# Kernel tuning notes

Measured on AMD Instinct MI355X. Metric: run time of the kernel, lower is better.

The kernel has to match this reference:

```python
import jax, jax.numpy as jnp
import numpy as np

B, S, E, D = 8, 2048, 512, 512  # batch, seq (mesh edges), elem_size, embd_size


def setup_inputs() -> dict:
    key = jax.random.key(0)
    ks = jax.random.split(key, 5)
    scale = 1.0 / np.sqrt(E)
    return {
        "x": jax.random.normal(ks[0], (B, S, E), dtype=jnp.float32),
        "Wq": jax.random.normal(ks[1], (E, D), dtype=jnp.float32) * scale,
        "bq": jax.random.normal(ks[2], (D,), dtype=jnp.float32) * 0.01,
        "Wk": jax.random.normal(ks[3], (E, D), dtype=jnp.float32) * scale,
        "bk": jax.random.normal(ks[4], (D,), dtype=jnp.float32) * 0.01,
    }


def reference(x, Wq, bq, Wk, bk):
    elem_size = x.shape[-1]
    q = jax.nn.relu(x @ Wq + bq)              # [B,S,D]
    k = jax.nn.relu(x @ Wk + bk)              # [B,S,D]
    scores = jnp.einsum("bqd,bkd->bqk", q, k) / (elem_size ** 0.5)  # [B,S,S]
    # nn.Softmax(dim=1): normalize over the QUERY axis (column-wise softmax)
    attn = jax.nn.softmax(scores, axis=1)
    new_values = jnp.einsum("bqk,bke->bqe", attn, x)  # V = raw x (use_V=False)
    return x + new_values                     # residual connection
```

## Files before the change

### kernel.cpp

```cpp
#include <hip/hip_runtime.h>
#include <hip/hip_bf16.h>
#include <math.h>

#define Bb 8
#define Ss 2048
#define Ee 512
#define Dd 512
#define QSPLIT 16

typedef __bf16 bf16x8 __attribute__((ext_vector_type(8)));
typedef __bf16 bf16x4 __attribute__((ext_vector_type(4)));
typedef float f32x4 __attribute__((ext_vector_type(4)));

__device__ __forceinline__ void stage_async(ushort* lds, const __bf16* gbase,
                                            int ldg, int wave, int lane) {
#pragma unroll
    for (int t = 0; t < 2; ++t) {
        const int idx = wave * 2 + t;
        const int row = idx * 16 + (lane >> 2);
        const int q8  = (((lane & 3) ^ ((lane >> 3) & 3)) * 8);
        __builtin_amdgcn_global_load_lds(
            (const __attribute__((address_space(1))) void*)(gbase + (size_t)row * ldg + q8),
            (__attribute__((address_space(3))) void*)(lds + idx * 512),
            16, 0, 0);
    }
}

__global__ void prep_x(const float* __restrict__ in, __bf16* __restrict__ xb,
                       __bf16* __restrict__ xT) {
    __shared__ float tile[32][33];
    const int b  = blockIdx.z;
    const int e0 = blockIdx.x * 32;
    const int s0 = blockIdx.y * 32;
    const float* ip = in + (size_t)b * Ss * Ee;
    __bf16* xbp = xb + (size_t)b * Ss * Ee;
    __bf16* xTp = xT + (size_t)b * Ee * Ss;
    for (int i = threadIdx.y; i < 32; i += 8) {
        const float v = ip[(size_t)(s0 + i) * Ee + e0 + threadIdx.x];
        tile[i][threadIdx.x] = v;
        xbp[(size_t)(s0 + i) * Ee + e0 + threadIdx.x] = (__bf16)v;
    }
    __syncthreads();
    for (int i = threadIdx.y; i < 32; i += 8)
        xTp[(size_t)(e0 + i) * Ss + s0 + threadIdx.x] = (__bf16)tile[threadIdx.x][i];
}

__global__ void transpose_w(const float* __restrict__ Wq, const float* __restrict__ Wk,
                            __bf16* __restrict__ WqT, __bf16* __restrict__ WkT) {
    __shared__ float tile[32][33];
    const float* in = blockIdx.z ? Wk : Wq;
    __bf16* out = blockIdx.z ? WkT : WqT;
    const int x0 = blockIdx.x * 32;
    const int y0 = blockIdx.y * 32;
    for (int i = threadIdx.y; i < 32; i += 8)
        tile[i][threadIdx.x] = in[(size_t)(y0 + i) * 512 + (x0 + threadIdx.x)];
    __syncthreads();
    for (int i = threadIdx.y; i < 32; i += 8)
        out[(size_t)(x0 + i) * 512 + (y0 + threadIdx.x)] = (__bf16)tile[threadIdx.x][i];
}

__global__ __launch_bounds__(256, 4) void proj_kernel(
    const __bf16* __restrict__ X,
    const __bf16* __restrict__ WqT, const __bf16* __restrict__ WkT,
    const float* __restrict__ bq, const float* __restrict__ bk,
    __bf16* __restrict__ qb, __bf16* __restrict__ kb)
{
    __shared__ __align__(16) ushort As[128 * 32];
    __shared__ __align__(16) ushort Bs[128 * 32];
    const __bf16* WT  = blockIdx.z ? WkT : WqT;
    const float* bias = blockIdx.z ? bk : bq;
    __bf16* Out       = blockIdx.z ? kb : qb;

    const int tid = threadIdx.x;
    const int wave = tid >> 6, lane = tid & 63, quad = lane >> 4, l16 = lane & 15;
    const int wm = (wave >> 1) * 64, wn = (wave & 1) * 64;
    const int m0 = blockIdx.y * 128, n0 = blockIdx.x * 128;
    const int sw = (quad ^ ((l16 >> 1) & 3)) * 8;
    const int K = 512;

    f32x4 acc[4][4];
    f32x4 zero = {0.f, 0.f, 0.f, 0.f};
    for (int i = 0; i < 4; i++) for (int j = 0; j < 4; j++) acc[i][j] = zero;

    for (int k0 = 0; k0 < K; k0 += 32) {
        stage_async(As, X  + (size_t)m0 * K + k0, K, wave, lane);
        stage_async(Bs, WT + (size_t)n0 * K + k0, K, wave, lane);
        __syncthreads();
        bf16x8 af[4], bfr[4];
        for (int i = 0; i < 4; i++) af[i]  = *(bf16x8*)&As[(wm + i * 16 + l16) * 32 + sw];
        for (int j = 0; j < 4; j++) bfr[j] = *(bf16x8*)&Bs[(wn + j * 16 + l16) * 32 + sw];
        for (int i = 0; i < 4; i++)
            for (int j = 0; j < 4; j++)
                acc[i][j] = __builtin_amdgcn_mfma_f32_16x16x32_bf16(af[i], bfr[j], acc[i][j], 0, 0, 0);
        __syncthreads();
    }

    for (int i = 0; i < 4; i++) {
        const int row = m0 + wm + i * 16 + quad * 4;
        for (int j = 0; j < 4; j++) {
            const int col = n0 + wn + j * 16 + l16;
            const float bv = bias[col];
            for (int rr = 0; rr < 4; rr++) {
                float v = acc[i][j][rr] + bv;
                v = v > 0.f ? v : 0.f;
                Out[(size_t)(row + rr) * 512 + col] = (__bf16)v;
            }
        }
    }
}

__global__ __launch_bounds__(256, 4) void scores_kernel(
    const __bf16* __restrict__ Q,
    const __bf16* __restrict__ Km,
    __bf16* __restrict__ P,
    float* __restrict__ Mp,
    float* __restrict__ Lp)
{
    __shared__ __align__(16) ushort As[128 * 32];
    __shared__ __align__(16) ushort Bs[128 * 32];
    const int b = blockIdx.z;
    const __bf16* A  = Q  + (size_t)b * Ss * Dd;
    const __bf16* Bp = Km + (size_t)b * Ss * Dd;
    __bf16* C = P + (size_t)b * Ss * Ss;

    const int tid = threadIdx.x;
    const int wave = tid >> 6, lane = tid & 63, quad = lane >> 4, l16 = lane & 15;
    const int wm = (wave >> 1) * 64, wn = (wave & 1) * 64;
    const int m0 = blockIdx.y * 128, n0 = blockIdx.x * 128;
    const int sw = (quad ^ ((l16 >> 1) & 3)) * 8;
    const float scale = 0.044194173824159216f;

    f32x4 acc[4][4];
    f32x4 zero = {0.f, 0.f, 0.f, 0.f};
    for (int i = 0; i < 4; i++) for (int j = 0; j < 4; j++) acc[i][j] = zero;

    for (int k0 = 0; k0 < Dd; k0 += 32) {
        stage_async(As, A  + (size_t)m0 * Dd + k0, Dd, wave, lane);
        stage_async(Bs, Bp + (size_t)n0 * Dd + k0, Dd, wave, lane);
        __syncthreads();
        bf16x8 af[4], bfr[4];
        for (int i = 0; i < 4; i++) af[i]  = *(bf16x8*)&As[(wm + i * 16 + l16) * 32 + sw];
        for (int j = 0; j < 4; j++) bfr[j] = *(bf16x8*)&Bs[(wn + j * 16 + l16) * 32 + sw];
        for (int i = 0; i < 4; i++)
            for (int j = 0; j < 4; j++)
                acc[i][j] = __builtin_amdgcn_mfma_f32_16x16x32_bf16(af[i], bfr[j], acc[i][j], 0, 0, 0);
        __syncthreads();
    }

    float* Ms = (float*)As;
    float* Ls = ((float*)As) + 256;
    const int half = wave >> 1;
    float mj[4];
    for (int j = 0; j < 4; j++) {
        float m = -1e30f;
        for (int i = 0; i < 4; i++)
            for (int rr = 0; rr < 4; rr++)
                m = fmaxf(m, acc[i][j][rr]);
        m = fmaxf(m, __shfl_xor(m, 16));
        m = fmaxf(m, __shfl_xor(m, 32));
        mj[j] = m;
    }
    if (quad == 0)
        for (int j = 0; j < 4; j++) Ms[half * 128 + wn + j * 16 + l16] = mj[j];
    __syncthreads();
    float mt[4];
    for (int j = 0; j < 4; j++) {
        const int c = wn + j * 16 + l16;
        mt[j] = fmaxf(Ms[c], Ms[128 + c]);
    }
    float lj[4];
    for (int j = 0; j < 4; j++) {
        const int col = n0 + wn + j * 16 + l16;
        float l = 0.f;
        for (int i = 0; i < 4; i++) {
            const int row = m0 + wm + i * 16 + quad * 4;
            for (int rr = 0; rr < 4; rr++) {
                const float e = __expf((acc[i][j][rr] - mt[j]) * scale);
                C[(size_t)(row + rr) * Ss + col] = (__bf16)e;
                l += e;
            }
        }
        l += __shfl_xor(l, 16);
        l += __shfl_xor(l, 32);
        lj[j] = l;
    }
    if (quad == 0)
        for (int j = 0; j < 4; j++) Ls[half * 128 + wn + j * 16 + l16] = lj[j];
    __syncthreads();
    if (tid < 128) {
        const size_t o = ((size_t)blockIdx.y * Bb + b) * Ss + n0 + tid;
        Mp[o] = fmaxf(Ms[tid], Ms[128 + tid]) * scale;
        Lp[o] = Ls[tid] + Ls[128 + tid];
    }
}

__global__ void stats_combine(const float* __restrict__ Mp, const float* __restrict__ Lp,
                              float* __restrict__ Mf, float* __restrict__ Li) {
    const int idx = blockIdx.x * 256 + threadIdx.x;
    float m = -1e30f;
    for (int qy = 0; qy < QSPLIT; qy++) m = fmaxf(m, Mp[(size_t)qy * Bb * Ss + idx]);
    float l = 0.f;
    for (int qy = 0; qy < QSPLIT; qy++)
        l += Lp[(size_t)qy * Bb * Ss + idx] * __expf(Mp[(size_t)qy * Bb * Ss + idx] - m);
    Mf[idx] = m;
    Li[idx] = 1.0f / l;
}

__global__ __launch_bounds__(256, 4) void pv_kernel(
    const __bf16* __restrict__ P,
    const float* __restrict__ Mp,
    const float* __restrict__ Mf,
    const float* __restrict__ Li,
    const __bf16* __restrict__ XT,
    const __bf16* __restrict__ XB,
    float* __restrict__ Out)
{
    __shared__ __align__(16) ushort As[128 * 32];
    __shared__ __align__(16) ushort Bs[128 * 32];
    __shared__ float corr[Ss];
    const int b = blockIdx.z;
    const int m0 = blockIdx.y * 128, n0 = blockIdx.x * 128;
    const int qy = blockIdx.y;
    const __bf16* A  = P  + (size_t)b * Ss * Ss;
    const __bf16* Bp = XT + (size_t)b * Ee * Ss;

    const int tid = threadIdx.x;
    const int wave = tid >> 6, lane = tid & 63, quad = lane >> 4, l16 = lane & 15;
    const int wm = (wave >> 1) * 64, wn = (wave & 1) * 64;
    const int sw = (quad ^ ((l16 >> 1) & 3)) * 8;
    const int r = tid >> 2, seg = (tid & 3) * 8;
    const int p8 = (((tid & 3) ^ ((r >> 1) & 3)) * 8);

    for (int k = tid; k < Ss; k += 256) {
        const float mp = Mp[((size_t)qy * Bb + b) * Ss + k];
        corr[k] = __expf(mp - Mf[(size_t)b * Ss + k]) * Li[(size_t)b * Ss + k];
    }
    __syncthreads();

    f32x4 acc[4][4];
    f32x4 zero = {0.f, 0.f, 0.f, 0.f};
    for (int i = 0; i < 4; i++) for (int j = 0; j < 4; j++) acc[i][j] = zero;

    for (int k0 = 0; k0 < Ss; k0 += 32) {
        float cv[8];
        #pragma unroll
        for (int t = 0; t < 8; t++) cv[t] = corr[k0 + seg + t];
        #pragma unroll
        for (int half = 0; half < 2; half++) {
            const int row = r + half * 64;
            const bf16x8 p = *(const bf16x8*)&A[(size_t)(m0 + row) * Ss + k0 + seg];
            bf16x8 o;
            #pragma unroll
            for (int t = 0; t < 8; t++) o[t] = (__bf16)((float)p[t] * cv[t]);
            *(bf16x8*)&As[row * 32 + p8] = o;
        }
        stage_async(Bs, Bp + (size_t)n0 * Ss + k0, Ss, wave, lane);
        __syncthreads();
        bf16x8 af[4], bfr[4];
        for (int i = 0; i < 4; i++) af[i]  = *(bf16x8*)&As[(wm + i * 16 + l16) * 32 + sw];
        for (int j = 0; j < 4; j++) bfr[j] = *(bf16x8*)&Bs[(wn + j * 16 + l16) * 32 + sw];
        for (int i = 0; i < 4; i++)
            for (int j = 0; j < 4; j++)
                acc[i][j] = __builtin_amdgcn_mfma_f32_16x16x32_bf16(af[i], bfr[j], acc[i][j], 0, 0, 0);
        __syncthreads();
    }

    for (int i = 0; i < 4; i++) {
        const int row = m0 + wm + i * 16 + quad * 4;
        for (int j = 0; j < 4; j++) {
            const int col = wn + j * 16 + l16 + n0;
            for (int rr = 0; rr < 4; rr++) {
                const size_t idx = ((size_t)b * Ss + row + rr) * Ee + col;
                Out[idx] = (float)XB[idx] + acc[i][j][rr];
            }
        }
    }
}

extern "C" void kernel_launch(void* const* d_in, const int* in_sizes, int n_in,
                              void* d_out, int out_size, void* d_ws, size_t ws_size,
                              hipStream_t stream) {
    const float* x  = (const float*)d_in[0];
    const float* Wq = (const float*)d_in[1];
    const float* bq = (const float*)d_in[2];
    const float* Wk = (const float*)d_in[3];
    const float* bk = (const float*)d_in[4];
    float* out = (float*)d_out;

    char* ws = (char*)d_ws;
    size_t off = 0;
    auto alloc = [&](size_t bytes) -> void* {
        void* p = ws + off;
        off += (bytes + 255) & ~(size_t)255;
        return p;
    };
    __bf16* P   = (__bf16*)alloc((size_t)Bb * Ss * Ss * 2);
    __bf16* xb  = (__bf16*)alloc((size_t)Bb * Ss * Ee * 2);
    __bf16* qb  = (__bf16*)alloc((size_t)Bb * Ss * Dd * 2);
    __bf16* kb  = (__bf16*)alloc((size_t)Bb * Ss * Dd * 2);
    __bf16* xT  = (__bf16*)alloc((size_t)Bb * Ee * Ss * 2);
    __bf16* WqT = (__bf16*)alloc((size_t)512 * 512 * 2);
    __bf16* WkT = (__bf16*)alloc((size_t)512 * 512 * 2);
    float*  Mp  = (float*)alloc((size_t)QSPLIT * Bb * Ss * 4);
    float*  Lp  = (float*)alloc((size_t)QSPLIT * Bb * Ss * 4);
    float*  Mf  = (float*)alloc((size_t)Bb * Ss * 4);
    float*  Li  = (float*)alloc((size_t)Bb * Ss * 4);
    if (off > ws_size) return;

    prep_x<<<dim3(16, 64, 8), dim3(32, 8), 0, stream>>>(x, xb, xT);
    transpose_w<<<dim3(16, 16, 2), dim3(32, 8), 0, stream>>>(Wq, Wk, WqT, WkT);

    proj_kernel<<<dim3(4, 128, 2), 256, 0, stream>>>(xb, WqT, WkT, bq, bk, qb, kb);

    scores_kernel<<<dim3(16, 16, 8), 256, 0, stream>>>(qb, kb, P, Mp, Lp);
    stats_combine<<<dim3(Bb * Ss / 256), 256, 0, stream>>>(Mp, Lp, Mf, Li);

    pv_kernel<<<dim3(4, 16, 8), 256, 0, stream>>>(P, Mp, Mf, Li, xT, xb, out);
}
```

Baseline: 239.8 us.

## Flatten grids with batch-fastest block order and prefetch P rows in pv_kernel

Both scores_kernel and pv_kernel now run on a 1D grid whose block index is decoded with the batch index varying fastest. Consecutive blocks therefore land on different batches, which likely spreads them across XCDs/L2 slices and changes which Q/K/P tiles are cached together. pv_kernel also register-prefetches the next k-slice of P before the MFMA loop and issues the async X^T staging earlier, so global loads overlap compute. The costs are extra register pressure and a wrapped (redundant) load on the last iteration.

```diff
diff --git a/kernel.cpp b/kernel.cpp
--- a/kernel.cpp
+++ b/kernel.cpp
@@ -118,7 +118,12 @@
 {
     __shared__ __align__(16) ushort As[128 * 32];
     __shared__ __align__(16) ushort Bs[128 * 32];
-    const int b = blockIdx.z;
+    const int id = blockIdx.x;
+    const int b = id & 7;
+    const int rest = id >> 3;
+    const int qy = rest >> 4;
+    const int m0 = qy * 128;
+    const int n0 = (rest & 15) * 128;
     const __bf16* A  = Q  + (size_t)b * Ss * Dd;
     const __bf16* Bp = Km + (size_t)b * Ss * Dd;
     __bf16* C = P + (size_t)b * Ss * Ss;
@@ -126,7 +131,6 @@
     const int tid = threadIdx.x;
     const int wave = tid >> 6, lane = tid & 63, quad = lane >> 4, l16 = lane & 15;
     const int wm = (wave >> 1) * 64, wn = (wave & 1) * 64;
-    const int m0 = blockIdx.y * 128, n0 = blockIdx.x * 128;
     const int sw = (quad ^ ((l16 >> 1) & 3)) * 8;
     const float scale = 0.044194173824159216f;
 
@@ -188,7 +192,7 @@
         for (int j = 0; j < 4; j++) Ls[half * 128 + wn + j * 16 + l16] = lj[j];
     __syncthreads();
     if (tid < 128) {
-        const size_t o = ((size_t)blockIdx.y * Bb + b) * Ss + n0 + tid;
+        const size_t o = ((size_t)qy * Bb + b) * Ss + n0 + tid;
         Mp[o] = fmaxf(Ms[tid], Ms[128 + tid]) * scale;
         Lp[o] = Ls[tid] + Ls[128 + tid];
     }
@@ -218,9 +222,12 @@
     __shared__ __align__(16) ushort As[128 * 32];
     __shared__ __align__(16) ushort Bs[128 * 32];
     __shared__ float corr[Ss];
-    const int b = blockIdx.z;
-    const int m0 = blockIdx.y * 128, n0 = blockIdx.x * 128;
-    const int qy = blockIdx.y;
+    const int id = blockIdx.x;
+    const int b = id & 7;
+    const int rest = id >> 3;
+    const int qy = rest >> 2;
+    const int m0 = qy * 128;
+    const int n0 = (rest & 3) * 128;
     const __bf16* A  = P  + (size_t)b * Ss * Ss;
     const __bf16* Bp = XT + (size_t)b * Ee * Ss;
 
@@ -241,24 +248,30 @@
     f32x4 zero = {0.f, 0.f, 0.f, 0.f};
     for (int i = 0; i < 4; i++) for (int j = 0; j < 4; j++) acc[i][j] = zero;
 
+    const __bf16* Arow0 = A + (size_t)(m0 + r) * Ss;
+    const __bf16* Arow1 = A + (size_t)(m0 + r + 64) * Ss;
+    bf16x8 pr0 = *(const bf16x8*)&Arow0[seg];
+    bf16x8 pr1 = *(const bf16x8*)&Arow1[seg];
+
     for (int k0 = 0; k0 < Ss; k0 += 32) {
+        stage_async(Bs, Bp + (size_t)n0 * Ss + k0, Ss, wave, lane);
         float cv[8];
         #pragma unroll
         for (int t = 0; t < 8; t++) cv[t] = corr[k0 + seg + t];
+        bf16x8 o0, o1;
         #pragma unroll
-        for (int half = 0; half < 2; half++) {
-            const int row = r + half * 64;
-            const bf16x8 p = *(const bf16x8*)&A[(size_t)(m0 + row) * Ss + k0 + seg];
-            bf16x8 o;
-            #pragma unroll
-            for (int t = 0; t < 8; t++) o[t] = (__bf16)((float)p[t] * cv[t]);
-            *(bf16x8*)&As[row * 32 + p8] = o;
-        }
-        stage_async(Bs, Bp + (size_t)n0 * Ss + k0, Ss, wave, lane);
+        for (int t = 0; t < 8; t++) o0[t] = (__bf16)((float)pr0[t] * cv[t]);
+        #pragma unroll
+        for (int t = 0; t < 8; t++) o1[t] = (__bf16)((float)pr1[t] * cv[t]);
+        *(bf16x8*)&As[r * 32 + p8]        = o0;
+        *(bf16x8*)&As[(r + 64) * 32 + p8] = o1;
         __syncthreads();
         bf16x8 af[4], bfr[4];
         for (int i = 0; i < 4; i++) af[i]  = *(bf16x8*)&As[(wm + i * 16 + l16) * 32 + sw];
         for (int j = 0; j < 4; j++) bfr[j] = *(bf16x8*)&Bs[(wn + j * 16 + l16) * 32 + sw];
+        const int kn = (k0 + 32) & (Ss - 1);
+        pr0 = *(const bf16x8*)&Arow0[kn + seg];
+        pr1 = *(const bf16x8*)&Arow1[kn + seg];
         for (int i = 0; i < 4; i++)
             for (int j = 0; j < 4; j++)
                 acc[i][j] = __builtin_amdgcn_mfma_f32_16x16x32_bf16(af[i], bfr[j], acc[i][j], 0, 0, 0);
@@ -312,8 +325,8 @@
 
     proj_kernel<<<dim3(4, 128, 2), 256, 0, stream>>>(xb, WqT, WkT, bq, bk, qb, kb);
 
-    scores_kernel<<<dim3(16, 16, 8), 256, 0, stream>>>(qb, kb, P, Mp, Lp);
+    scores_kernel<<<dim3(2048), 256, 0, stream>>>(qb, kb, P, Mp, Lp);
     stats_combine<<<dim3(Bb * Ss / 256), 256, 0, stream>>>(Mp, Lp, Mf, Li);
 
-    pv_kernel<<<dim3(4, 16, 8), 256, 0, stream>>>(P, Mp, Mf, Li, xT, xb, out);
-}
+    pv_kernel<<<dim3(512), 256, 0, stream>>>(P, Mp, Mf, Li, xT, xb, out);
+}
```

Result: faster. 232.2 us (-3.2%).
